# Performance work log

Measured on AMD Instinct MI355X. Metric: run time of the kernel, lower is better.

The kernel has to match this reference:

```python
import jax, jax.numpy as jnp
import numpy as np

K = 3  # kernel_size
PAD = (K - 1) // 2


def _extract_patches(x):
    # x: (B, C, H, W) -> patches (B, C, K, K, H, W), matching F.unfold layout
    B, C, H, W = x.shape
    xp = jnp.pad(x, ((0, 0), (0, 0), (PAD, PAD), (PAD, PAD)))
    rows = []
    for dy in range(K):
        cols = [xp[:, :, dy:dy + H, dx:dx + W] for dx in range(K)]
        rows.append(jnp.stack(cols, axis=2))  # (B, C, K, H, W)
    return jnp.stack(rows, axis=2)  # (B, C, K, K, H, W)


def setup_inputs() -> dict:
    key = jax.random.key(0)
    k1, k2 = jax.random.split(key)
    B, Cin, Cout, Hs, Ws = 64, 64, 64, 64, 64
    x = jax.random.normal(k1, (B, Cin, Hs, Ws), dtype=jnp.float32)
    # weights: (h_size, w_size, out_channels, in_channels, K, K), scaled by 1/in_channels
    weights = jax.random.normal(k2, (Hs, Ws, Cout, Cin, K, K), dtype=jnp.float32) / Cin
    return {"x": x, "weights": weights}


def reference(x, weights):
    # Locally-connected conv: distinct (out,in,K,K) filter per spatial location.
    patches = _extract_patches(x)  # (B, in, K, K, h, w)
    # weights: i=h, j=w, a=out, b=in, c,d=K; patches: r=batch, b=in, c,d=K, i=h, j=w
    out = jnp.einsum('ijabcd,rbcdij->raij', weights, patches)  # (B, out, h, w)
    return jax.nn.relu(out)  # final_layer=False -> ReLU
```

## Files before the change

### kernel.cpp

```cpp
#include <hip/hip_runtime.h>

typedef short bf16x8 __attribute__((ext_vector_type(8)));
typedef float f32x4  __attribute__((ext_vector_type(4)));
typedef unsigned short u16x4 __attribute__((ext_vector_type(4)));

#define LSTR 296

__device__ __forceinline__ unsigned short f2bf(float f) {
    unsigned u = __float_as_uint(f);
    return (unsigned short)((u + 0x7FFFu + ((u >> 16) & 1u)) >> 16);
}

__global__ __launch_bounds__(256)
void transpose_in(const float* __restrict__ x, unsigned short* __restrict__ xT) {
    __shared__ float tile[64][65];
    const int t  = threadIdx.x;
    const int tr = blockIdx.x >> 6, tc = blockIdx.x & 63;
    const int r0 = tr << 6, c0 = tc << 6;
    const int cc = (t & 15) << 2;
    #pragma unroll
    for (int q = 0; q < 4; ++q) {
        const int rr = (t >> 4) + (q << 4);
        const f32x4 v = __builtin_nontemporal_load(
            (const f32x4*)&x[(size_t)(r0 + rr) * 4096 + c0 + cc]);
        tile[rr][cc + 0] = v[0]; tile[rr][cc + 1] = v[1];
        tile[rr][cc + 2] = v[2]; tile[rr][cc + 3] = v[3];
    }
    __syncthreads();
    #pragma unroll
    for (int q = 0; q < 4; ++q) {
        const int rr = (t >> 4) + (q << 4);
        u16x4 o;
        o[0] = f2bf(tile[cc + 0][rr]); o[1] = f2bf(tile[cc + 1][rr]);
        o[2] = f2bf(tile[cc + 2][rr]); o[3] = f2bf(tile[cc + 3][rr]);
        *(u16x4*)&xT[(size_t)(c0 + rr) * 4096 + r0 + cc] = o;
    }
}

__global__ __launch_bounds__(256)
void transpose_out(const float* __restrict__ src, float* __restrict__ dst) {
    __shared__ float tile[64][65];
    const int t  = threadIdx.x;
    const int tr = blockIdx.x >> 6, tc = blockIdx.x & 63;
    const int r0 = tr << 6, c0 = tc << 6;
    const int cc = (t & 15) << 2;
    #pragma unroll
    for (int q = 0; q < 4; ++q) {
        const int rr = (t >> 4) + (q << 4);
        const f32x4 v = __builtin_nontemporal_load(
            (const f32x4*)&src[(size_t)(r0 + rr) * 4096 + c0 + cc]);
        tile[rr][cc + 0] = v[0]; tile[rr][cc + 1] = v[1];
        tile[rr][cc + 2] = v[2]; tile[rr][cc + 3] = v[3];
    }
    __syncthreads();
    #pragma unroll
    for (int q = 0; q < 4; ++q) {
        const int rr = (t >> 4) + (q << 4);
        f32x4 o;
        o[0] = tile[cc + 0][rr]; o[1] = tile[cc + 1][rr];
        o[2] = tile[cc + 2][rr]; o[3] = tile[cc + 3][rr];
        *(f32x4*)&dst[(size_t)(c0 + rr) * 4096 + r0 + cc] = o;
    }
}

template <bool TO_OUTT>
__global__ __launch_bounds__(256, 4)
void lc_main(const unsigned short* __restrict__ xT, const float* __restrict__ wt,
             float* __restrict__ outp) {
    __shared__ __align__(16) unsigned short A[64 * LSTR];

    const int bid = blockIdx.x;
    const int swz = (bid & 7) * 512 + (bid >> 3);
    const int h   = swz >> 6;
    const int wq  = swz & 63;

    const int t    = threadIdx.x;
    const int lane = t & 63;
    const int wv   = t >> 6;

    const float* wloc = wt + (size_t)((h << 6) + wq) * 36864;
    const int co = (wv << 4) + (lane & 15);
    const int kg = lane >> 4;
    const float* wrow = wloc + co * 576 + (kg << 3);

    f32x4 acc[4] = {{0.f,0.f,0.f,0.f},{0.f,0.f,0.f,0.f},
                    {0.f,0.f,0.f,0.f},{0.f,0.f,0.f,0.f}};

    const int b_st = t >> 2;
    const int cig  = t & 3;

    for (int hs = 0; hs < 2; ++hs) {
        const int kbase = hs * 288;

        f32x4 pb[3][2];
        pb[0][0] = __builtin_nontemporal_load((const f32x4*)(wrow + kbase + 0));
        pb[0][1] = __builtin_nontemporal_load((const f32x4*)(wrow + kbase + 4));
        pb[1][0] = __builtin_nontemporal_load((const f32x4*)(wrow + kbase + 32));
        pb[1][1] = __builtin_nontemporal_load((const f32x4*)(wrow + kbase + 36));

        #pragma unroll
        for (int tap = 0; tap < 9; ++tap) {
            const int dy = tap / 3, dx = tap % 3;
            const int y  = h + dy - 1;
            const int xx = wq + dx - 1;
            bf16x8 v = {0,0,0,0,0,0,0,0};
            if ((unsigned)y < 64u && (unsigned)xx < 64u) {
                v = *(const bf16x8*)&xT[(size_t)((y << 6) + xx) * 4096
                                        + (b_st << 6) + (hs << 5) + (cig << 3)];
            }
            unsigned short* dst = &A[b_st * LSTR + cig * 72 + tap];
            #pragma unroll
            for (int j = 0; j < 8; ++j) dst[j * 9] = (unsigned short)v[j];
        }
        __syncthreads();

        #pragma unroll
        for (int ks = 0; ks < 9; ++ks) {
            const int cur = ks % 3;
            const int nxt = (ks + 2) % 3;
            if (ks < 7) {
                const float* np = wrow + kbase + (ks + 2) * 32;
                pb[nxt][0] = __builtin_nontemporal_load((const f32x4*)(np));
                pb[nxt][1] = __builtin_nontemporal_load((const f32x4*)(np + 4));
            }
            const f32x4 lo = pb[cur][0], hi = pb[cur][1];
            bf16x8 bf;
            bf[0] = (short)f2bf(lo[0]); bf[1] = (short)f2bf(lo[1]);
            bf[2] = (short)f2bf(lo[2]); bf[3] = (short)f2bf(lo[3]);
            bf[4] = (short)f2bf(hi[0]); bf[5] = (short)f2bf(hi[1]);
            bf[6] = (short)f2bf(hi[2]); bf[7] = (short)f2bf(hi[3]);
            const int kk = (ks << 5) + (kg << 3);
            #pragma unroll
            for (int mt = 0; mt < 4; ++mt) {
                const bf16x8 af = *(const bf16x8*)&A[((mt << 4) + (lane & 15)) * LSTR + kk];
                acc[mt] = __builtin_amdgcn_mfma_f32_16x16x32_bf16(af, bf, acc[mt], 0, 0, 0);
            }
        }
        __syncthreads();
    }

    const int rg = lane >> 4;
    if (TO_OUTT) {
        const size_t obase = (size_t)((h << 6) + wq) * 4096;
        #pragma unroll
        for (int mt = 0; mt < 4; ++mt) {
            #pragma unroll
            for (int j = 0; j < 4; ++j) {
                const int b = (mt << 4) + (rg << 2) + j;
                outp[obase + (b << 6) + co] = fmaxf(acc[mt][j], 0.f);
            }
        }
    } else {
        #pragma unroll
        for (int mt = 0; mt < 4; ++mt) {
            #pragma unroll
            for (int j = 0; j < 4; ++j) {
                const int b = (mt << 4) + (rg << 2) + j;
                outp[(size_t)((b << 6) + co) * 4096 + (h << 6) + wq] = fmaxf(acc[mt][j], 0.f);
            }
        }
    }
}

__global__ __launch_bounds__(256, 4)
void lc_mfma(const float* __restrict__ x, const float* __restrict__ wt,
             float* __restrict__ out) {
    __shared__ __align__(16) unsigned short A[64 * LSTR];
    const int bid = blockIdx.x;
    const int swz = (bid & 7) * 512 + (bid >> 3);
    const int h   = swz >> 6;
    const int wq  = swz & 63;
    const int t    = threadIdx.x;
    const int lane = t & 63;
    const int wv   = t >> 6;
    const float* wloc = wt + (size_t)((h << 6) + wq) * 36864;
    const int co = (wv << 4) + (lane & 15);
    const int kg = lane >> 4;
    const float* wrow = wloc + co * 576 + (kg << 3);
    f32x4 acc[4] = {{0.f,0.f,0.f,0.f},{0.f,0.f,0.f,0.f},
                    {0.f,0.f,0.f,0.f},{0.f,0.f,0.f,0.f}};
    const int cil = t & 31;
    const int bro = t >> 5;
    for (int hs = 0; hs < 2; ++hs) {
        const int kbase = hs * 288;
        f32x4 pb[3][2];
        pb[0][0] = __builtin_nontemporal_load((const f32x4*)(wrow + kbase + 0));
        pb[0][1] = __builtin_nontemporal_load((const f32x4*)(wrow + kbase + 4));
        pb[1][0] = __builtin_nontemporal_load((const f32x4*)(wrow + kbase + 32));
        pb[1][1] = __builtin_nontemporal_load((const f32x4*)(wrow + kbase + 36));
        {
            const int ci = (hs << 5) + cil;
            for (int p = 0; p < 8; ++p) {
                const int b = (p << 3) + bro;
                const float* xb = x + ((size_t)((b << 6) + ci) << 12);
                unsigned short* dst = &A[b * LSTR + cil * 9];
                #pragma unroll
                for (int dy = 0; dy < 3; ++dy) {
                    const int y = h + dy - 1;
                    const bool yok = (unsigned)y < 64u;
                    #pragma unroll
                    for (int dx = 0; dx < 3; ++dx) {
                        const int xx = wq + dx - 1;
                        float v = 0.f;
                        if (yok && (unsigned)xx < 64u) v = xb[(y << 6) + xx];
                        dst[dy * 3 + dx] = f2bf(v);
                    }
                }
            }
        }
        __syncthreads();
        #pragma unroll
        for (int ks = 0; ks < 9; ++ks) {
            const int cur = ks % 3;
            const int nxt = (ks + 2) % 3;
            if (ks < 7) {
                const float* np = wrow + kbase + (ks + 2) * 32;
                pb[nxt][0] = __builtin_nontemporal_load((const f32x4*)(np));
                pb[nxt][1] = __builtin_nontemporal_load((const f32x4*)(np + 4));
            }
            const f32x4 lo = pb[cur][0], hi = pb[cur][1];
            bf16x8 bf;
            bf[0] = (short)f2bf(lo[0]); bf[1] = (short)f2bf(lo[1]);
            bf[2] = (short)f2bf(lo[2]); bf[3] = (short)f2bf(lo[3]);
            bf[4] = (short)f2bf(hi[0]); bf[5] = (short)f2bf(hi[1]);
            bf[6] = (short)f2bf(hi[2]); bf[7] = (short)f2bf(hi[3]);
            const int kk = (ks << 5) + (kg << 3);
            #pragma unroll
            for (int mt = 0; mt < 4; ++mt) {
                const bf16x8 af = *(const bf16x8*)&A[((mt << 4) + (lane & 15)) * LSTR + kk];
                acc[mt] = __builtin_amdgcn_mfma_f32_16x16x32_bf16(af, bf, acc[mt], 0, 0, 0);
            }
        }
        __syncthreads();
    }
    const int rg = lane >> 4;
    #pragma unroll
    for (int mt = 0; mt < 4; ++mt) {
        #pragma unroll
        for (int j = 0; j < 4; ++j) {
            const int b = (mt << 4) + (rg << 2) + j;
            out[(size_t)((b << 6) + co) * 4096 + (h << 6) + wq] = fmaxf(acc[mt][j], 0.f);
        }
    }
}

extern "C" void kernel_launch(void* const* d_in, const int* in_sizes, int n_in,
                              void* d_out, int out_size, void* d_ws, size_t ws_size,
                              hipStream_t stream) {
    const float* x  = (const float*)d_in[0];
    const float* wt = (const float*)d_in[1];
    float* out = (float*)d_out;

    const size_t xT_bytes   = (size_t)4096 * 4096 * 2;
    const size_t outT_bytes = (size_t)4096 * 4096 * 4;

    if (ws_size >= xT_bytes + outT_bytes) {
        unsigned short* xT = (unsigned short*)d_ws;
        float* outT = (float*)((char*)d_ws + xT_bytes);
        hipLaunchKernelGGL(transpose_in, dim3(4096), dim3(256), 0, stream, x, xT);
        hipLaunchKernelGGL((lc_main<true>), dim3(4096), dim3(256), 0, stream, xT, wt, outT);
        hipLaunchKernelGGL(transpose_out, dim3(4096), dim3(256), 0, stream, outT, out);
    } else if (ws_size >= xT_bytes) {
        unsigned short* xT = (unsigned short*)d_ws;
        hipLaunchKernelGGL(transpose_in, dim3(4096), dim3(256), 0, stream, x, xT);
        hipLaunchKernelGGL((lc_main<false>), dim3(4096), dim3(256), 0, stream, xT, wt, out);
    } else {
        hipLaunchKernelGGL(lc_mfma, dim3(4096), dim3(256), 0, stream, x, wt, out);
    }
}
```

Before: 202.6 us.

## Store intermediate output as bf16 and prefetch second channel half during MMA

Result: no change. 200.2 us (-1.2%).

```diff
diff --git a/kernel.cpp b/kernel.cpp
--- a/kernel.cpp
+++ b/kernel.cpp
@@ -38,8 +38,8 @@
 }
 
 __global__ __launch_bounds__(256)
-void transpose_out(const float* __restrict__ src, float* __restrict__ dst) {
-    __shared__ float tile[64][65];
+void transpose_out_bf(const unsigned short* __restrict__ src, float* __restrict__ dst) {
+    __shared__ unsigned short tile[64][66];
     const int t  = threadIdx.x;
     const int tr = blockIdx.x >> 6, tc = blockIdx.x & 63;
     const int r0 = tr << 6, c0 = tc << 6;
@@ -47,8 +47,8 @@
     #pragma unroll
     for (int q = 0; q < 4; ++q) {
         const int rr = (t >> 4) + (q << 4);
-        const f32x4 v = __builtin_nontemporal_load(
-            (const f32x4*)&src[(size_t)(r0 + rr) * 4096 + c0 + cc]);
+        const u16x4 v = __builtin_nontemporal_load(
+            (const u16x4*)&src[(size_t)(r0 + rr) * 4096 + c0 + cc]);
         tile[rr][cc + 0] = v[0]; tile[rr][cc + 1] = v[1];
         tile[rr][cc + 2] = v[2]; tile[rr][cc + 3] = v[3];
     }
@@ -57,16 +57,17 @@
     for (int q = 0; q < 4; ++q) {
         const int rr = (t >> 4) + (q << 4);
         f32x4 o;
-        o[0] = tile[cc + 0][rr]; o[1] = tile[cc + 1][rr];
-        o[2] = tile[cc + 2][rr]; o[3] = tile[cc + 3][rr];
-        *(f32x4*)&dst[(size_t)(c0 + rr) * 4096 + r0 + cc] = o;
-    }
-}
-
-template <bool TO_OUTT>
+        o[0] = __uint_as_float((unsigned)tile[cc + 0][rr] << 16);
+        o[1] = __uint_as_float((unsigned)tile[cc + 1][rr] << 16);
+        o[2] = __uint_as_float((unsigned)tile[cc + 2][rr] << 16);
+        o[3] = __uint_as_float((unsigned)tile[cc + 3][rr] << 16);
+        __builtin_nontemporal_store(o, (f32x4*)&dst[(size_t)(c0 + rr) * 4096 + r0 + cc]);
+    }
+}
+
 __global__ __launch_bounds__(256, 4)
 void lc_main(const unsigned short* __restrict__ xT, const float* __restrict__ wt,
-             float* __restrict__ outp) {
+             unsigned short* __restrict__ outT) {
     __shared__ __align__(16) unsigned short A[64 * LSTR];
 
     const int bid = blockIdx.x;
@@ -89,75 +90,80 @@
     const int b_st = t >> 2;
     const int cig  = t & 3;
 
-    for (int hs = 0; hs < 2; ++hs) {
-        const int kbase = hs * 288;
-
-        f32x4 pb[3][2];
-        pb[0][0] = __builtin_nontemporal_load((const f32x4*)(wrow + kbase + 0));
-        pb[0][1] = __builtin_nontemporal_load((const f32x4*)(wrow + kbase + 4));
-        pb[1][0] = __builtin_nontemporal_load((const f32x4*)(wrow + kbase + 32));
-        pb[1][1] = __builtin_nontemporal_load((const f32x4*)(wrow + kbase + 36));
-
-        #pragma unroll
-        for (int tap = 0; tap < 9; ++tap) {
-            const int dy = tap / 3, dx = tap % 3;
-            const int y  = h + dy - 1;
-            const int xx = wq + dx - 1;
-            bf16x8 v = {0,0,0,0,0,0,0,0};
-            if ((unsigned)y < 64u && (unsigned)xx < 64u) {
-                v = *(const bf16x8*)&xT[(size_t)((y << 6) + xx) * 4096
-                                        + (b_st << 6) + (hs << 5) + (cig << 3)];
-            }
-            unsigned short* dst = &A[b_st * LSTR + cig * 72 + tap];
+    f32x4 pb[3][2];
+    pb[0][0] = __builtin_nontemporal_load((const f32x4*)(wrow + 0));
+    pb[0][1] = __builtin_nontemporal_load((const f32x4*)(wrow + 4));
+    pb[1][0] = __builtin_nontemporal_load((const f32x4*)(wrow + 32));
+    pb[1][1] = __builtin_nontemporal_load((const f32x4*)(wrow + 36));
+
+    bf16x8 xr[9];
+    #pragma unroll
+    for (int tap = 0; tap < 9; ++tap) {
+        const int y  = h + tap / 3 - 1;
+        const int xx = wq + tap % 3 - 1;
+        bf16x8 v = {0,0,0,0,0,0,0,0};
+        if ((unsigned)y < 64u && (unsigned)xx < 64u)
+            v = *(const bf16x8*)&xT[(size_t)((y << 6) + xx) * 4096 + (b_st << 6) + (cig << 3)];
+        xr[tap] = v;
+    }
+    {
+        unsigned short* dst = &A[b_st * LSTR + cig * 72];
+        #pragma unroll
+        for (int tap = 0; tap < 9; ++tap)
             #pragma unroll
-            for (int j = 0; j < 8; ++j) dst[j * 9] = (unsigned short)v[j];
-        }
-        __syncthreads();
-
-        #pragma unroll
-        for (int ks = 0; ks < 9; ++ks) {
-            const int cur = ks % 3;
-            const int nxt = (ks + 2) % 3;
-            if (ks < 7) {
-                const float* np = wrow + kbase + (ks + 2) * 32;
-                pb[nxt][0] = __builtin_nontemporal_load((const f32x4*)(np));
-                pb[nxt][1] = __builtin_nontemporal_load((const f32x4*)(np + 4));
-            }
-            const f32x4 lo = pb[cur][0], hi = pb[cur][1];
-            bf16x8 bf;
-            bf[0] = (short)f2bf(lo[0]); bf[1] = (short)f2bf(lo[1]);
-            bf[2] = (short)f2bf(lo[2]); bf[3] = (short)f2bf(lo[3]);
-            bf[4] = (short)f2bf(hi[0]); bf[5] = (short)f2bf(hi[1]);
-            bf[6] = (short)f2bf(hi[2]); bf[7] = (short)f2bf(hi[3]);
-            const int kk = (ks << 5) + (kg << 3);
+            for (int j = 0; j < 8; ++j)
+                dst[j * 9 + tap] = (unsigned short)xr[tap][j];
+    }
+    #pragma unroll
+    for (int tap = 0; tap < 9; ++tap) {
+        const int y  = h + tap / 3 - 1;
+        const int xx = wq + tap % 3 - 1;
+        bf16x8 v = {0,0,0,0,0,0,0,0};
+        if ((unsigned)y < 64u && (unsigned)xx < 64u)
+            v = *(const bf16x8*)&xT[(size_t)((y << 6) + xx) * 4096 + (b_st << 6) + 32 + (cig << 3)];
+        xr[tap] = v;
+    }
+    __syncthreads();
+
+    #pragma unroll
+    for (int ks = 0; ks < 18; ++ks) {
+        if (ks == 9) {
+            __syncthreads();
+            unsigned short* dst = &A[b_st * LSTR + cig * 72];
             #pragma unroll
-            for (int mt = 0; mt < 4; ++mt) {
-                const bf16x8 af = *(const bf16x8*)&A[((mt << 4) + (lane & 15)) * LSTR + kk];
-                acc[mt] = __builtin_amdgcn_mfma_f32_16x16x32_bf16(af, bf, acc[mt], 0, 0, 0);
-            }
-        }
-        __syncthreads();
+            for (int tap = 0; tap < 9; ++tap)
+                #pragma unroll
+                for (int j = 0; j < 8; ++j)
+                    dst[j * 9 + tap] = (unsigned short)xr[tap][j];
+            __syncthreads();
+        }
+        if (ks < 16) {
+            const float* np = wrow + (ks + 2) * 32;
+            pb[(ks + 2) % 3][0] = __builtin_nontemporal_load((const f32x4*)(np));
+            pb[(ks + 2) % 3][1] = __builtin_nontemporal_load((const f32x4*)(np + 4));
+        }
+        const f32x4 lo = pb[ks % 3][0], hi = pb[ks % 3][1];
+        bf16x8 bf;
+        bf[0] = (short)f2bf(lo[0]); bf[1] = (short)f2bf(lo[1]);
+        bf[2] = (short)f2bf(lo[2]); bf[3] = (short)f2bf(lo[3]);
+        bf[4] = (short)f2bf(hi[0]); bf[5] = (short)f2bf(hi[1]);
+        bf[6] = (short)f2bf(hi[2]); bf[7] = (short)f2bf(hi[3]);
+        const int kk = (ks % 9) * 32 + (kg << 3);
+        #pragma unroll
+        for (int mt = 0; mt < 4; ++mt) {
+            const bf16x8 af = *(const bf16x8*)&A[((mt << 4) + (lane & 15)) * LSTR + kk];
+            acc[mt] = __builtin_amdgcn_mfma_f32_16x16x32_bf16(af, bf, acc[mt], 0, 0, 0);
+        }
     }
 
     const int rg = lane >> 4;
-    if (TO_OUTT) {
-        const size_t obase = (size_t)((h << 6) + wq) * 4096;
-        #pragma unroll
-        for (int mt = 0; mt < 4; ++mt) {
-            #pragma unroll
-            for (int j = 0; j < 4; ++j) {
-                const int b = (mt << 4) + (rg << 2) + j;
-                outp[obase + (b << 6) + co] = fmaxf(acc[mt][j], 0.f);
-            }
-        }
-    } else {
-        #pragma unroll
-        for (int mt = 0; mt < 4; ++mt) {
-            #pragma unroll
-            for (int j = 0; j < 4; ++j) {
-                const int b = (mt << 4) + (rg << 2) + j;
-                outp[(size_t)((b << 6) + co) * 4096 + (h << 6) + wq] = fmaxf(acc[mt][j], 0.f);
-            }
+    const size_t obase = (size_t)((h << 6) + wq) * 4096;
+    #pragma unroll
+    for (int mt = 0; mt < 4; ++mt) {
+        #pragma unroll
+        for (int j = 0; j < 4; ++j) {
+            const int b = (mt << 4) + (rg << 2) + j;
+            outT[obase + (b << 6) + co] = f2bf(fmaxf(acc[mt][j], 0.f));
         }
     }
 }
@@ -252,18 +258,14 @@
     float* out = (float*)d_out;
 
     const size_t xT_bytes   = (size_t)4096 * 4096 * 2;
-    const size_t outT_bytes = (size_t)4096 * 4096 * 4;
+    const size_t outT_bytes = (size_t)4096 * 4096 * 2;
 
     if (ws_size >= xT_bytes + outT_bytes) {
-        unsigned short* xT = (unsigned short*)d_ws;
-        float* outT = (float*)((char*)d_ws + xT_bytes);
+        unsigned short* xT   = (unsigned short*)d_ws;
+        unsigned short* outT = (unsigned short*)((char*)d_ws + xT_bytes);
         hipLaunchKernelGGL(transpose_in, dim3(4096), dim3(256), 0, stream, x, xT);
-        hipLaunchKernelGGL((lc_main<true>), dim3(4096), dim3(256), 0, stream, xT, wt, outT);
-        hipLaunchKernelGGL(transpose_out, dim3(4096), dim3(256), 0, stream, outT, out);
-    } else if (ws_size >= xT_bytes) {
-        unsigned short* xT = (unsigned short*)d_ws;
-        hipLaunchKernelGGL(transpose_in, dim3(4096), dim3(256), 0, stream, x, xT);
-        hipLaunchKernelGGL((lc_main<false>), dim3(4096), dim3(256), 0, stream, xT, wt, out);
+        hipLaunchKernelGGL(lc_main, dim3(4096), dim3(256), 0, stream, xT, wt, outT);
+        hipLaunchKernelGGL(transpose_out_bf, dim3(4096), dim3(256), 0, stream, outT, out);
     } else {
         hipLaunchKernelGGL(lc_mfma, dim3(4096), dim3(256), 0, stream, x, wt, out);
     }
```
